# Kernel optimization log

Hardware: AMD Instinct MI355X
Metric: run time of the kernel (lower is better)

The kernel has to match this reference:

```python
import jax, jax.numpy as jnp
import numpy as np

EPS_MIN = 1e-8
N_ITER = 50  # solver_iter


def solve_qp_simplex(M, n_iter=N_ITER):
    """Frank-Wolfe min over the simplex of alpha^T M alpha. M: (B,K,K) -> alpha: (B,K)."""
    B, K, _ = M.shape
    alpha0 = jnp.full((B, K), 1.0 / K, dtype=M.dtype)

    def step(alpha, it):
        grad = 2.0 * jnp.einsum('bij,bj->bi', M, alpha)           # (B,K)
        idx = jnp.argmin(grad, axis=1)                             # (B,)
        s = jax.nn.one_hot(idx, K, dtype=alpha.dtype)              # vertex of simplex
        gamma = 2.0 / (it + 2.0)
        return (1.0 - gamma) * alpha + gamma * s, None

    alpha, _ = jax.lax.scan(step, alpha0, jnp.arange(n_iter, dtype=M.dtype))
    return alpha


def _raw_loss(scores, targets, C):
    B, K = scores.shape
    # epsilon = offdiag_mean of C per batch, scaled by 1.0, clamped
    offdiag_mean = (C.sum(axis=(1, 2)) - jnp.trace(C, axis1=1, axis2=2)) / (K * K - K)
    eps = jnp.maximum(offdiag_mean, EPS_MIN)                       # (B,)

    f = 0.5 * scores
    exponent = -(f[:, :, None] + f[:, None, :] + C) / eps[:, None, None]  # (B,K,K)
    shift = exponent.max(axis=(1, 2), keepdims=True)
    logM = exponent - shift
    M = jnp.exp(logM)

    # solver is an implicit layer: non-differentiable by construction
    alpha = jax.lax.stop_gradient(solve_qp_simplex(M, N_ITER))     # (B,K)

    pos = alpha > 0
    loga = jnp.where(pos, jnp.log(jnp.where(pos, alpha, 1.0)), -jnp.inf)
    term = loga[:, :, None] + loga[:, None, :] + logM              # (B,K,K)
    logval = jax.scipy.special.logsumexp(term.reshape(B, K * K), axis=1)
    conjugate = -eps * (logval + shift.reshape(B))

    f_y = jnp.take_along_axis(scores, targets[:, None], axis=1)[:, 0]
    return conjugate - f_y


def setup_inputs() -> dict:
    key = jax.random.key(0)
    k1, k2, k3 = jax.random.split(key, 3)
    B, K = 512, 256
    scores = jax.random.normal(k1, (B, K), dtype=jnp.float32)
    targets = jax.random.randint(k2, (B,), 0, K)
    C = jax.random.uniform(k3, (B, K, K), dtype=jnp.float32)
    return {"scores": scores, "targets": targets, "C": C}


def reference(scores, targets, C):
    return _raw_loss(scores, targets, C).mean()
```

## Files before the change

### kernel.cpp

```cpp
#include <hip/hip_runtime.h>
#include <math.h>

#define KDIM 256
#define NITER 50


__global__ __launch_bounds__(256) void k1_partials(
    const float* __restrict__ scores, const float* __restrict__ C,
    float* __restrict__ psum_o, float* __restrict__ ptrace_o, float* __restrict__ pmin_o)
{
    const int blk = blockIdx.x;
    const int b = blk >> 2, chunk = blk & 3;
    const int tid = threadIdx.x, lane = tid & 63, wave = tid >> 6;
    const float4* C4 = (const float4*)(C + (size_t)b * KDIM * KDIM);

    __shared__ float4 sf4[KDIM/4];
    __shared__ float redS[256], redT[256], redM[256];
    const float* sf = (const float*)sf4;
    ((float*)sf4)[tid] = 0.5f * scores[b*KDIM + tid];
    __syncthreads();

    const int row0 = chunk * 64;
    float psum = 0.f, ptrace = 0.f, pmin = INFINITY;
    #pragma unroll
    for (int rr = 0; rr < 16; ++rr) {
        const int row = row0 + wave + rr*4;
        float4 c4 = C4[row*(KDIM/4) + lane];
        float frow = sf[row];
        float4 fj = sf4[lane];
        psum += (c4.x + c4.y) + (c4.z + c4.w);
        pmin = fminf(pmin, fminf(fminf(frow+fj.x+c4.x, frow+fj.y+c4.y),
                                 fminf(frow+fj.z+c4.z, frow+fj.w+c4.w)));
        if ((row >> 2) == lane) {
            int r2 = row & 3;
            ptrace += (r2==0) ? c4.x : (r2==1) ? c4.y : (r2==2) ? c4.z : c4.w;
        }
    }
    redS[tid] = psum; redT[tid] = ptrace; redM[tid] = pmin;
    __syncthreads();
    for (int s = 128; s > 0; s >>= 1) {
        if (tid < s) {
            redS[tid] += redS[tid+s];
            redT[tid] += redT[tid+s];
            redM[tid]  = fminf(redM[tid], redM[tid+s]);
        }
        __syncthreads();
    }
    if (tid == 0) { psum_o[blk] = redS[0]; ptrace_o[blk] = redT[0]; pmin_o[blk] = redM[0]; }
}

__global__ __launch_bounds__(256) void k2_grad0(
    const float* __restrict__ scores, const float* __restrict__ C,
    const float* __restrict__ psum_i, const float* __restrict__ ptrace_i, const float* __restrict__ pmin_i,
    float* __restrict__ rsval_o, int* __restrict__ rsidx_o)
{
    const int blk = blockIdx.x;
    const int b = blk >> 2, chunk = blk & 3;
    const int tid = threadIdx.x, lane = tid & 63, wave = tid >> 6;
    const float4* C4 = (const float4*)(C + (size_t)b * KDIM * KDIM);

    __shared__ float4 sf4[KDIM/4];
    __shared__ float rs64[64];
    const float* sf = (const float*)sf4;
    ((float*)sf4)[tid] = 0.5f * scores[b*KDIM + tid];
    __syncthreads();

    float sum = 0.f, tr = 0.f, mn = INFINITY;
    #pragma unroll
    for (int c2 = 0; c2 < 4; ++c2) {
        sum += psum_i[b*4 + c2];
        tr  += ptrace_i[b*4 + c2];
        mn   = fminf(mn, pmin_i[b*4 + c2]);
    }
    const float eps = fmaxf((sum - tr) / (float)(KDIM*KDIM - KDIM), 1e-8f);
    const float inv_eps = 1.0f / eps;
    const float minv = mn;

    const int row0 = chunk * 64;
    for (int rr = wave; rr < 64; rr += 4) {
        const int row = row0 + rr;
        float4 c4 = C4[row*(KDIM/4) + lane];
        float frow = sf[row];
        float4 fj = sf4[lane];
        float p = __expf((minv - (frow+fj.x+c4.x)) * inv_eps)
                + __expf((minv - (frow+fj.y+c4.y)) * inv_eps)
                + __expf((minv - (frow+fj.z+c4.z)) * inv_eps)
                + __expf((minv - (frow+fj.w+c4.w)) * inv_eps);
        for (int off = 32; off > 0; off >>= 1) p += __shfl_xor(p, off);
        if (lane == 0) rs64[rr] = p;
    }
    __syncthreads();
    if (wave == 0) {
        float v = rs64[lane]; int vi = row0 + lane;
        for (int off = 32; off > 0; off >>= 1) {
            float ov = __shfl_xor(v, off);
            int  ovi = __shfl_xor(vi, off);
            if (ov < v || (ov == v && ovi < vi)) { v = ov; vi = ovi; }
        }
        if (lane == 0) { rsval_o[blk] = v; rsidx_o[blk] = vi; }
    }
}

__global__ __launch_bounds__(256) void k3_fw(
    const float* __restrict__ scores, const int* __restrict__ targets,
    const float* __restrict__ C,
    const float* __restrict__ psum_i, const float* __restrict__ ptrace_i, const float* __restrict__ pmin_i,
    const float* __restrict__ rsval_i, const int* __restrict__ rsidx_i,
    float* __restrict__ lossB)
{
    const int b = blockIdx.x;
    const int tid = threadIdx.x, lane = tid & 63, wave = tid >> 6;
    const float* Cb = C + (size_t)b * KDIM * KDIM;

    __shared__ float4 sf4[KDIM/4];
    __shared__ float aAll[KDIM];
    __shared__ float wm[4], wsm[4];
    __shared__ int   wcnt[4];
    __shared__ int   sIdx[64];
    __shared__ float sLog[64];

    const float* sf = (const float*)sf4;
    ((float*)sf4)[tid] = 0.5f * scores[b*KDIM + tid];
    __syncthreads();

    float sum = 0.f, tr = 0.f, mn = INFINITY;
    #pragma unroll
    for (int c2 = 0; c2 < 4; ++c2) {
        sum += psum_i[b*4 + c2];
        tr  += ptrace_i[b*4 + c2];
        mn   = fminf(mn, pmin_i[b*4 + c2]);
    }
    const float eps = fmaxf((sum - tr) / (float)(KDIM*KDIM - KDIM), 1e-8f);
    const float inv_eps = 1.0f / eps;
    const float minv = mn;

    float bv = INFINITY; int idx0 = 0;
    #pragma unroll
    for (int c2 = 0; c2 < 4; ++c2) {
        float v = rsval_i[b*4 + c2];
        int  vi = rsidx_i[b*4 + c2];
        if (v < bv) { bv = v; idx0 = vi; }
    }

    if (wave == 0) {
        const float f0 = sf[lane], f1 = sf[lane+64], f2 = sf[lane+128], f3 = sf[lane+192];
        const float* r0 = Cb + (size_t)lane*KDIM;
        const float* r1 = r0 + 64*KDIM;
        const float* r2 = r0 + 128*KDIM;
        const float* r3 = r0 + 192*KDIM;

        float fidx = sf[idx0];
        float g0 = 2.0f * __expf((minv - (f0 + fidx + r0[idx0])) * inv_eps);
        float g1 = 2.0f * __expf((minv - (f1 + fidx + r1[idx0])) * inv_eps);
        float g2 = 2.0f * __expf((minv - (f2 + fidx + r2[idx0])) * inv_eps);
        float g3 = 2.0f * __expf((minv - (f3 + fidx + r3[idx0])) * inv_eps);
        float a0 = (lane     == idx0) ? 1.0f : 0.0f;
        float a1 = (lane+64  == idx0) ? 1.0f : 0.0f;
        float a2 = (lane+128 == idx0) ? 1.0f : 0.0f;
        float a3 = (lane+192 == idx0) ? 1.0f : 0.0f;

        for (int it = 1; it < NITER; ++it) {
            float v = g0; int vi = lane;
            if (g1 < v) { v = g1; vi = lane+64; }
            if (g2 < v) { v = g2; vi = lane+128; }
            if (g3 < v) { v = g3; vi = lane+192; }
            #pragma unroll
            for (int off = 32; off > 0; off >>= 1) {
                float ov = __shfl_xor(v, off);
                int  ovi = __shfl_xor(vi, off);
                if (ov < v || (ov == v && ovi < vi)) { v = ov; vi = ovi; }
            }
            const int idx = vi;
            const float gamma = 2.0f / ((float)it + 2.0f);
            const float omg = 1.0f - gamma;
            fidx = sf[idx];
            const float c0 = r0[idx], c1 = r1[idx], c2_ = r2[idx], c3 = r3[idx];
            g0 = omg*g0 + 2.0f*gamma*__expf((minv - (f0 + fidx + c0)) * inv_eps);
            g1 = omg*g1 + 2.0f*gamma*__expf((minv - (f1 + fidx + c1)) * inv_eps);
            g2 = omg*g2 + 2.0f*gamma*__expf((minv - (f2 + fidx + c2_)) * inv_eps);
            g3 = omg*g3 + 2.0f*gamma*__expf((minv - (f3 + fidx + c3)) * inv_eps);
            a0 = omg*a0 + ((lane     == idx) ? gamma : 0.0f);
            a1 = omg*a1 + ((lane+64  == idx) ? gamma : 0.0f);
            a2 = omg*a2 + ((lane+128 == idx) ? gamma : 0.0f);
            a3 = omg*a3 + ((lane+192 == idx) ? gamma : 0.0f);
        }
        aAll[lane]     = a0;
        aAll[lane+64]  = a1;
        aAll[lane+128] = a2;
        aAll[lane+192] = a3;
    }
    __syncthreads();

    const float a = aAll[tid];

    unsigned long long mask = __ballot(a > 0.f);
    if (lane == 0) wcnt[wave] = __popcll(mask);
    __syncthreads();
    int off0 = 0;
    for (int w = 0; w < wave; ++w) off0 += wcnt[w];
    const int count = wcnt[0] + wcnt[1] + wcnt[2] + wcnt[3];
    if (a > 0.f) {
        int pos = off0 + __popcll(mask & ((1ull << lane) - 1ull));
        sIdx[pos] = tid;
        sLog[pos] = logf(a);
    }
    __syncthreads();

    float m = -INFINITY, ss = 0.f;
    const int total = count * count;
    for (int p = tid; p < total; p += KDIM) {
        int ii = p / count;
        int jj = p - ii * count;
        int i = sIdx[ii], j = sIdx[jj];
        float cij = Cb[i*KDIM + j];
        float lm = (minv - (sf[i] + sf[j] + cij)) * inv_eps;
        float t = sLog[ii] + sLog[jj] + lm;
        if (t > m) { ss = ss * __expf(m - t) + 1.0f; m = t; }
        else       { ss += __expf(t - m); }
    }
    #pragma unroll
    for (int off = 32; off > 0; off >>= 1) {
        float om = __shfl_xor(m, off);
        float os = __shfl_xor(ss, off);
        if (os > 0.f) {
            if (ss <= 0.f)   { m = om; ss = os; }
            else if (om > m) { ss = ss*__expf(m-om) + os; m = om; }
            else             { ss += os*__expf(om-m); }
        }
    }
    if (lane == 0) { wm[wave] = m; wsm[wave] = ss; }
    __syncthreads();
    if (tid == 0) {
        float M = wm[0], S = wsm[0];
        #pragma unroll
        for (int w = 1; w < 4; ++w) {
            float om = wm[w], os = wsm[w];
            if (os > 0.f) {
                if (S <= 0.f)    { M = om; S = os; }
                else if (om > M) { S = S*__expf(M-om) + os; M = om; }
                else             { S += os*__expf(om-M); }
            }
        }
        float logval = M + logf(S);
        float shift = -minv * inv_eps;
        float conjugate = -eps * (logval + shift);
        float fy = scores[b*KDIM + targets[b]];
        lossB[b] = conjugate - fy;
    }
}

__global__ __launch_bounds__(512) void cacis_reduce(const float* __restrict__ lossB,
                                                    float* __restrict__ out, int B)
{
    __shared__ float red[512];
    int t = threadIdx.x;
    red[t] = (t < B) ? lossB[t] : 0.f;
    __syncthreads();
    for (int s = 256; s > 0; s >>= 1) { if (t < s) red[t] += red[t+s]; __syncthreads(); }
    if (t == 0) out[0] = red[0] / (float)B;
}

extern "C" void kernel_launch(void* const* d_in, const int* in_sizes, int n_in,
                              void* d_out, int out_size, void* d_ws, size_t ws_size,
                              hipStream_t stream) {
    const float* scores  = (const float*)d_in[0];
    const int*   targets = (const int*)d_in[1];
    const float* C       = (const float*)d_in[2];
    float* out = (float*)d_out;
    const int B = in_sizes[1];

    float* ws     = (float*)d_ws;
    float* psum   = ws;
    float* ptrace = ws + 2048;
    float* pmin   = ws + 4096;
    float* rsval  = ws + 6144;
    int*   rsidx  = (int*)(ws + 8192);
    float* lossB  = ws + 10240;

    k1_partials<<<B*4, 256, 0, stream>>>(scores, C, psum, ptrace, pmin);
    k2_grad0   <<<B*4, 256, 0, stream>>>(scores, C, psum, ptrace, pmin, rsval, rsidx);
    k3_fw      <<<B,   256, 0, stream>>>(scores, targets, C, psum, ptrace, pmin, rsval, rsidx, lossB);
    cacis_reduce<<<1, 512, 0, stream>>>(lossB, out, B);
}
```

Baseline: 112.1 us.

## Fuse partial-reduction, gradient-init and Frank-Wolfe kernels via last-block-done counter

Merges the three per-batch kernels into one launch: each of the four chunk blocks writes its partial sums and bumps a per-batch atomic counter, and the last block to finish computes eps and the initial gradient over the whole matrix, then runs the Frank-Wolfe solve and the logsumexp. Block indices are remapped so the chunks of one batch run close together and the C rows are likely still in cache. It also swaps an LDS read of f[idx] for a wave shuffle inside the solver loop. In exchange, the finishing block now does the full 256-row gradient-init pass alone, a memset is added, and the serial tail per batch gets longer.

```diff
diff --git a/kernel.cpp b/kernel.cpp
--- a/kernel.cpp
+++ b/kernel.cpp
@@ -5,17 +5,30 @@
 #define NITER 50
 
 
-__global__ __launch_bounds__(256) void k1_partials(
-    const float* __restrict__ scores, const float* __restrict__ C,
+__global__ __launch_bounds__(256) void cacis_fused(
+    const float* __restrict__ scores, const int* __restrict__ targets,
+    const float* __restrict__ C,
+    int* __restrict__ cnt, float* __restrict__ lossB,
     float* __restrict__ psum_o, float* __restrict__ ptrace_o, float* __restrict__ pmin_o)
 {
-    const int blk = blockIdx.x;
-    const int b = blk >> 2, chunk = blk & 3;
+    const int B0 = blockIdx.x;
+    const int b = ((B0 >> 5) << 3) | (B0 & 7);
+    const int chunk = (B0 >> 3) & 3;
     const int tid = threadIdx.x, lane = tid & 63, wave = tid >> 6;
-    const float4* C4 = (const float4*)(C + (size_t)b * KDIM * KDIM);
+    const float* Cb = C + (size_t)b * KDIM * KDIM;
+    const float4* C4 = (const float4*)Cb;
 
     __shared__ float4 sf4[KDIM/4];
     __shared__ float redS[256], redT[256], redM[256];
+    __shared__ float rs[KDIM];
+    __shared__ float aAll[KDIM];
+    __shared__ float bcast[2];
+    __shared__ int   iret;
+    __shared__ int   wcnt[4];
+    __shared__ int   sIdx[64];
+    __shared__ float sLog[64];
+    __shared__ float wm[4], wsm[4];
+
     const float* sf = (const float*)sf4;
     ((float*)sf4)[tid] = 0.5f * scores[b*KDIM + tid];
     __syncthreads();
@@ -46,39 +59,35 @@
         }
         __syncthreads();
     }
-    if (tid == 0) { psum_o[blk] = redS[0]; ptrace_o[blk] = redT[0]; pmin_o[blk] = redM[0]; }
-}
-
-__global__ __launch_bounds__(256) void k2_grad0(
-    const float* __restrict__ scores, const float* __restrict__ C,
-    const float* __restrict__ psum_i, const float* __restrict__ ptrace_i, const float* __restrict__ pmin_i,
-    float* __restrict__ rsval_o, int* __restrict__ rsidx_o)
-{
-    const int blk = blockIdx.x;
-    const int b = blk >> 2, chunk = blk & 3;
-    const int tid = threadIdx.x, lane = tid & 63, wave = tid >> 6;
-    const float4* C4 = (const float4*)(C + (size_t)b * KDIM * KDIM);
-
-    __shared__ float4 sf4[KDIM/4];
-    __shared__ float rs64[64];
-    const float* sf = (const float*)sf4;
-    ((float*)sf4)[tid] = 0.5f * scores[b*KDIM + tid];
-    __syncthreads();
-
-    float sum = 0.f, tr = 0.f, mn = INFINITY;
-    #pragma unroll
-    for (int c2 = 0; c2 < 4; ++c2) {
-        sum += psum_i[b*4 + c2];
-        tr  += ptrace_i[b*4 + c2];
-        mn   = fminf(mn, pmin_i[b*4 + c2]);
-    }
-    const float eps = fmaxf((sum - tr) / (float)(KDIM*KDIM - KDIM), 1e-8f);
+    if (tid == 0) {
+        const int slot = b*4 + chunk;
+        __hip_atomic_store(&psum_o[slot],   redS[0], __ATOMIC_RELAXED, __HIP_MEMORY_SCOPE_AGENT);
+        __hip_atomic_store(&ptrace_o[slot], redT[0], __ATOMIC_RELAXED, __HIP_MEMORY_SCOPE_AGENT);
+        __hip_atomic_store(&pmin_o[slot],   redM[0], __ATOMIC_RELAXED, __HIP_MEMORY_SCOPE_AGENT);
+        iret = __hip_atomic_fetch_add(&cnt[b], 1, __ATOMIC_ACQ_REL, __HIP_MEMORY_SCOPE_AGENT);
+    }
+    __syncthreads();
+    if (iret != 3) return;
+
+    if (tid == 0) {
+        float sum = 0.f, tr = 0.f, mn = INFINITY;
+        #pragma unroll
+        for (int k2 = 0; k2 < 4; ++k2) {
+            sum += __hip_atomic_load(&psum_o[b*4+k2],   __ATOMIC_RELAXED, __HIP_MEMORY_SCOPE_AGENT);
+            tr  += __hip_atomic_load(&ptrace_o[b*4+k2], __ATOMIC_RELAXED, __HIP_MEMORY_SCOPE_AGENT);
+            mn   = fminf(mn, __hip_atomic_load(&pmin_o[b*4+k2], __ATOMIC_RELAXED, __HIP_MEMORY_SCOPE_AGENT));
+        }
+        bcast[0] = mn;
+        bcast[1] = fmaxf((sum - tr) / (float)(KDIM*KDIM - KDIM), 1e-8f);
+    }
+    __syncthreads();
+    const float minv = bcast[0];
+    const float eps = bcast[1];
     const float inv_eps = 1.0f / eps;
-    const float minv = mn;
-
-    const int row0 = chunk * 64;
-    for (int rr = wave; rr < 64; rr += 4) {
-        const int row = row0 + rr;
+
+    #pragma unroll 4
+    for (int rr = 0; rr < 64; ++rr) {
+        const int row = rr*4 + wave;
         float4 c4 = C4[row*(KDIM/4) + lane];
         float frow = sf[row];
         float4 fj = sf4[lane];
@@ -86,61 +95,11 @@
                 + __expf((minv - (frow+fj.y+c4.y)) * inv_eps)
                 + __expf((minv - (frow+fj.z+c4.z)) * inv_eps)
                 + __expf((minv - (frow+fj.w+c4.w)) * inv_eps);
+        #pragma unroll
         for (int off = 32; off > 0; off >>= 1) p += __shfl_xor(p, off);
-        if (lane == 0) rs64[rr] = p;
-    }
-    __syncthreads();
-    if (wave == 0) {
-        float v = rs64[lane]; int vi = row0 + lane;
-        for (int off = 32; off > 0; off >>= 1) {
-            float ov = __shfl_xor(v, off);
-            int  ovi = __shfl_xor(vi, off);
-            if (ov < v || (ov == v && ovi < vi)) { v = ov; vi = ovi; }
-        }
-        if (lane == 0) { rsval_o[blk] = v; rsidx_o[blk] = vi; }
-    }
-}
-
-__global__ __launch_bounds__(256) void k3_fw(
-    const float* __restrict__ scores, const int* __restrict__ targets,
-    const float* __restrict__ C,
-    const float* __restrict__ psum_i, const float* __restrict__ ptrace_i, const float* __restrict__ pmin_i,
-    const float* __restrict__ rsval_i, const int* __restrict__ rsidx_i,
-    float* __restrict__ lossB)
-{
-    const int b = blockIdx.x;
-    const int tid = threadIdx.x, lane = tid & 63, wave = tid >> 6;
-    const float* Cb = C + (size_t)b * KDIM * KDIM;
-
-    __shared__ float4 sf4[KDIM/4];
-    __shared__ float aAll[KDIM];
-    __shared__ float wm[4], wsm[4];
-    __shared__ int   wcnt[4];
-    __shared__ int   sIdx[64];
-    __shared__ float sLog[64];
-
-    const float* sf = (const float*)sf4;
-    ((float*)sf4)[tid] = 0.5f * scores[b*KDIM + tid];
-    __syncthreads();
-
-    float sum = 0.f, tr = 0.f, mn = INFINITY;
-    #pragma unroll
-    for (int c2 = 0; c2 < 4; ++c2) {
-        sum += psum_i[b*4 + c2];
-        tr  += ptrace_i[b*4 + c2];
-        mn   = fminf(mn, pmin_i[b*4 + c2]);
-    }
-    const float eps = fmaxf((sum - tr) / (float)(KDIM*KDIM - KDIM), 1e-8f);
-    const float inv_eps = 1.0f / eps;
-    const float minv = mn;
-
-    float bv = INFINITY; int idx0 = 0;
-    #pragma unroll
-    for (int c2 = 0; c2 < 4; ++c2) {
-        float v = rsval_i[b*4 + c2];
-        int  vi = rsidx_i[b*4 + c2];
-        if (v < bv) { bv = v; idx0 = vi; }
-    }
+        if (lane == 0) rs[row] = p;
+    }
+    __syncthreads();
 
     if (wave == 0) {
         const float f0 = sf[lane], f1 = sf[lane+64], f2 = sf[lane+128], f3 = sf[lane+192];
@@ -148,6 +107,19 @@
         const float* r1 = r0 + 64*KDIM;
         const float* r2 = r0 + 128*KDIM;
         const float* r3 = r0 + 192*KDIM;
+
+        float v = rs[lane]; int vi = lane;
+        float t;
+        t = rs[lane+64];  if (t < v) { v = t; vi = lane+64; }
+        t = rs[lane+128]; if (t < v) { v = t; vi = lane+128; }
+        t = rs[lane+192]; if (t < v) { v = t; vi = lane+192; }
+        #pragma unroll
+        for (int off = 32; off > 0; off >>= 1) {
+            float ov = __shfl_xor(v, off);
+            int  ovi = __shfl_xor(vi, off);
+            if (ov < v || (ov == v && ovi < vi)) { v = ov; vi = ovi; }
+        }
+        const int idx0 = vi;
 
         float fidx = sf[idx0];
         float g0 = 2.0f * __expf((minv - (f0 + fidx + r0[idx0])) * inv_eps);
@@ -160,25 +132,27 @@
         float a3 = (lane+192 == idx0) ? 1.0f : 0.0f;
 
         for (int it = 1; it < NITER; ++it) {
-            float v = g0; int vi = lane;
-            if (g1 < v) { v = g1; vi = lane+64; }
-            if (g2 < v) { v = g2; vi = lane+128; }
-            if (g3 < v) { v = g3; vi = lane+192; }
+            float v2 = g0; int vi2 = lane;
+            if (g1 < v2) { v2 = g1; vi2 = lane+64; }
+            if (g2 < v2) { v2 = g2; vi2 = lane+128; }
+            if (g3 < v2) { v2 = g3; vi2 = lane+192; }
             #pragma unroll
             for (int off = 32; off > 0; off >>= 1) {
-                float ov = __shfl_xor(v, off);
-                int  ovi = __shfl_xor(vi, off);
-                if (ov < v || (ov == v && ovi < vi)) { v = ov; vi = ovi; }
+                float ov = __shfl_xor(v2, off);
+                int  ovi = __shfl_xor(vi2, off);
+                if (ov < v2 || (ov == v2 && ovi < vi2)) { v2 = ov; vi2 = ovi; }
             }
-            const int idx = vi;
+            const int idx = vi2;
             const float gamma = 2.0f / ((float)it + 2.0f);
             const float omg = 1.0f - gamma;
-            fidx = sf[idx];
+            const int which = idx >> 6;
+            float fsel = (which==0) ? f0 : (which==1) ? f1 : (which==2) ? f2 : f3;
+            const float fidx2 = __shfl(fsel, idx & 63);
             const float c0 = r0[idx], c1 = r1[idx], c2_ = r2[idx], c3 = r3[idx];
-            g0 = omg*g0 + 2.0f*gamma*__expf((minv - (f0 + fidx + c0)) * inv_eps);
-            g1 = omg*g1 + 2.0f*gamma*__expf((minv - (f1 + fidx + c1)) * inv_eps);
-            g2 = omg*g2 + 2.0f*gamma*__expf((minv - (f2 + fidx + c2_)) * inv_eps);
-            g3 = omg*g3 + 2.0f*gamma*__expf((minv - (f3 + fidx + c3)) * inv_eps);
+            g0 = omg*g0 + 2.0f*gamma*__expf((minv - (f0 + fidx2 + c0)) * inv_eps);
+            g1 = omg*g1 + 2.0f*gamma*__expf((minv - (f1 + fidx2 + c1)) * inv_eps);
+            g2 = omg*g2 + 2.0f*gamma*__expf((minv - (f2 + fidx2 + c2_)) * inv_eps);
+            g3 = omg*g3 + 2.0f*gamma*__expf((minv - (f3 + fidx2 + c3)) * inv_eps);
             a0 = omg*a0 + ((lane     == idx) ? gamma : 0.0f);
             a1 = omg*a1 + ((lane+64  == idx) ? gamma : 0.0f);
             a2 = omg*a2 + ((lane+128 == idx) ? gamma : 0.0f);
@@ -214,9 +188,9 @@
         int i = sIdx[ii], j = sIdx[jj];
         float cij = Cb[i*KDIM + j];
         float lm = (minv - (sf[i] + sf[j] + cij)) * inv_eps;
-        float t = sLog[ii] + sLog[jj] + lm;
-        if (t > m) { ss = ss * __expf(m - t) + 1.0f; m = t; }
-        else       { ss += __expf(t - m); }
+        float tt = sLog[ii] + sLog[jj] + lm;
+        if (tt > m) { ss = ss * __expf(m - tt) + 1.0f; m = tt; }
+        else        { ss += __expf(tt - m); }
     }
     #pragma unroll
     for (int off = 32; off > 0; off >>= 1) {
@@ -270,15 +244,13 @@
     const int B = in_sizes[1];
 
     float* ws     = (float*)d_ws;
-    float* psum   = ws;
-    float* ptrace = ws + 2048;
-    float* pmin   = ws + 4096;
-    float* rsval  = ws + 6144;
-    int*   rsidx  = (int*)(ws + 8192);
-    float* lossB  = ws + 10240;
-
-    k1_partials<<<B*4, 256, 0, stream>>>(scores, C, psum, ptrace, pmin);
-    k2_grad0   <<<B*4, 256, 0, stream>>>(scores, C, psum, ptrace, pmin, rsval, rsidx);
-    k3_fw      <<<B,   256, 0, stream>>>(scores, targets, C, psum, ptrace, pmin, rsval, rsidx, lossB);
+    int*   cnt    = (int*)ws;
+    float* lossB  = ws + 512;
+    float* psum   = ws + 1024;
+    float* ptrace = ws + 3072;
+    float* pmin   = ws + 5120;
+
+    hipMemsetAsync(cnt, 0, B * sizeof(int), stream);
+    cacis_fused<<<B*4, 256, 0, stream>>>(scores, targets, C, cnt, lossB, psum, ptrace, pmin);
     cacis_reduce<<<1, 512, 0, stream>>>(lossB, out, B);
 }
```

New measurement: 217.0 us. 93.5% more time.
